# Performance work log

Hardware: AMD Instinct MI355X
Metric: run time of the kernel (lower is better)

Reference implementation:

```python
import jax, jax.numpy as jnp
import numpy as np

EPS = 1e-5

def gcn_conv(x, src, dst, W, b, N):
    # PyG GCNConv with self-loops already appended to (src, dst):
    # out = D^{-1/2} (A+I) D^{-1/2} (x @ W) + b
    h = x @ W  # [N, F_out]
    deg = jax.ops.segment_sum(jnp.ones(dst.shape[0], h.dtype), dst, num_segments=N)
    dinv = jnp.where(deg > 0, jax.lax.rsqrt(deg), 0.0)
    norm = dinv[src] * dinv[dst]  # [E']
    msg = h[src] * norm[:, None]  # gather + scale
    out = jax.ops.segment_sum(msg, dst, num_segments=N)  # scatter-add
    return out + b

def layer_norm(x, gamma, beta):
    mu = jnp.mean(x, axis=-1, keepdims=True)
    var = jnp.mean((x - mu) ** 2, axis=-1, keepdims=True)
    return (x - mu) * jax.lax.rsqrt(var + EPS) * gamma + beta

def setup_inputs() -> dict:
    key = jax.random.key(0)
    ks = jax.random.split(key, 12)
    N, E, STEPS = 200000, 12800000, 4
    node = jax.random.normal(ks[0], (N, 3), dtype=jnp.float32)
    edges = jax.random.randint(ks[1], (2, E), 0, N, dtype=jnp.int64)
    W1 = jax.random.normal(ks[2], (3, 6), dtype=jnp.float32) * 0.5
    b1 = jnp.zeros((6,), jnp.float32)
    Wl = jax.random.normal(ks[3], (STEPS, 6, 6), dtype=jnp.float32) * 0.4
    bl = jnp.zeros((STEPS, 6), jnp.float32)
    gamma = jnp.ones((STEPS, 6), jnp.float32)
    beta = jnp.zeros((STEPS, 6), jnp.float32)
    Wfc = jax.random.normal(ks[4], (6, 3), dtype=jnp.float32) * 0.4
    bfc = jnp.zeros((3,), jnp.float32)
    return {"node": node, "edges": edges, "W1": W1, "b1": b1, "Wl": Wl,
            "bl": bl, "gamma": gamma, "beta": beta, "Wfc": Wfc, "bfc": bfc}

def reference(node, edges, W1, b1, Wl, bl, gamma, beta, Wfc, bfc):
    N = node.shape[0]
    loops = jnp.arange(N, dtype=edges.dtype)
    src = jnp.concatenate([edges[0], loops])  # add self-loops once
    dst = jnp.concatenate([edges[1], loops])
    x = gcn_conv(node, src, dst, W1, b1, N)
    steps = Wl.shape[0]
    for i in range(steps):
        x_res = x
        x = gcn_conv(x, src, dst, Wl[i], bl[i], N)
        x = layer_norm(x, gamma[i], beta[i])
        x = x + x_res
        x = jax.nn.relu(x)
    return x @ Wfc + bfc
```

## Files before the change

### kernel.cpp

```cpp
#include <hip/hip_runtime.h>
#include <hip/hip_fp16.h>
#include <cstdint>

#define EPSLN 1e-5f
#define NPB 256
#define NPB_SHIFT 8
#define MAXB 1024
#define TILE 16384
#define SRC_BITS 18
#define SRC_MASK 0x3FFFF
#define FCAP 17664
#define FK 35

__global__ __launch_bounds__(512) void k_init(int* __restrict__ bcur, int B, int cap) {
    int b = blockIdx.x * 512 + threadIdx.x;
    if (b < B) bcur[b] = b * cap;
}

__global__ __launch_bounds__(512) void k_scatter(const int* __restrict__ src,
                                                 const int* __restrict__ dst,
                                                 int* __restrict__ bcur,
                                                 unsigned* __restrict__ packed,
                                                 int E, int B) {
    __shared__ unsigned stg[TILE];
    __shared__ int hist[MAXB];
    __shared__ int lbase[MAXB + 1];
    __shared__ int sm[MAXB];
    int tid = threadIdx.x;
    int i0 = tid, i1 = tid + 512;
    hist[i0] = 0; hist[i1] = 0;
    __syncthreads();

    int beg = blockIdx.x * TILE;
    int end = min(beg + TILE, E);
    int cnt = end - beg;

    unsigned w[32];
    unsigned m[32];

    if (cnt == TILE && ((E & 3) == 0)) {
        const int4* d4 = (const int4*)(dst + beg);
        const int4* s4 = (const int4*)(src + beg);
#pragma unroll
        for (int k = 0; k < 8; ++k) {
            int4 d = d4[tid + k * 512];
            int4 s = s4[tid + k * 512];
            int b0 = d.x >> NPB_SHIFT, b1 = d.y >> NPB_SHIFT;
            int b2 = d.z >> NPB_SHIFT, b3 = d.w >> NPB_SHIFT;
            int r0 = atomicAdd(&hist[b0], 1);
            int r1 = atomicAdd(&hist[b1], 1);
            int r2 = atomicAdd(&hist[b2], 1);
            int r3 = atomicAdd(&hist[b3], 1);
            w[4 * k + 0] = ((unsigned)(d.x & (NPB - 1)) << SRC_BITS) | (unsigned)s.x;
            w[4 * k + 1] = ((unsigned)(d.y & (NPB - 1)) << SRC_BITS) | (unsigned)s.y;
            w[4 * k + 2] = ((unsigned)(d.z & (NPB - 1)) << SRC_BITS) | (unsigned)s.z;
            w[4 * k + 3] = ((unsigned)(d.w & (NPB - 1)) << SRC_BITS) | (unsigned)s.w;
            m[4 * k + 0] = ((unsigned)b0 << 14) | (unsigned)r0;
            m[4 * k + 1] = ((unsigned)b1 << 14) | (unsigned)r1;
            m[4 * k + 2] = ((unsigned)b2 << 14) | (unsigned)r2;
            m[4 * k + 3] = ((unsigned)b3 << 14) | (unsigned)r3;
        }
    } else {
#pragma unroll
        for (int k = 0; k < 32; ++k) {
            int i = beg + tid + k * 512;
            if (i < end) {
                int d = dst[i];
                int s = src[i];
                int bkt = d >> NPB_SHIFT;
                int r = atomicAdd(&hist[bkt], 1);
                w[k] = ((unsigned)(d & (NPB - 1)) << SRC_BITS) | (unsigned)s;
                m[k] = ((unsigned)bkt << 14) | (unsigned)r;
            } else {
                m[k] = 0xFFFFFFFFu;
            }
        }
    }
    __syncthreads();

    int v0 = hist[i0], v1 = hist[i1];
    sm[i0] = v0; sm[i1] = v1;
    __syncthreads();
    for (int off = 1; off < MAXB; off <<= 1) {
        int t0 = (i0 >= off) ? sm[i0 - off] : 0;
        int t1 = (i1 >= off) ? sm[i1 - off] : 0;
        __syncthreads();
        sm[i0] += t0; sm[i1] += t1;
        __syncthreads();
    }
    lbase[i0] = sm[i0] - v0;
    lbase[i1] = sm[i1] - v1;
    if (i0 < B) hist[i0] = v0 ? atomicAdd(&bcur[i0], v0) : 0;
    if (i1 < B) hist[i1] = v1 ? atomicAdd(&bcur[i1], v1) : 0;
    if (tid == 0) lbase[B] = cnt;
    __syncthreads();

#pragma unroll
    for (int k = 0; k < 32; ++k) {
        if (m[k] != 0xFFFFFFFFu) {
            int bkt = (int)(m[k] >> 14);
            int r   = (int)(m[k] & 16383u);
            stg[lbase[bkt] + r] = w[k];
        }
    }
    __syncthreads();

    int wv = tid >> 6;
    int ln = tid & 63;
    for (int b = wv; b < B; b += 8) {
        int lb = lbase[b];
        int le = lbase[b + 1];
        int gb = hist[b];
        for (int j = lb + ln; j < le; j += 64)
            packed[gb + (j - lb)] = stg[j];
    }
}

__global__ __launch_bounds__(512) void k_fine(const int* __restrict__ bcur,
                                              const unsigned* __restrict__ packed,
                                              int* __restrict__ csr,
                                              int2* __restrict__ ptr2,
                                              float* __restrict__ dinv,
                                              float* __restrict__ sqd,
                                              const float* __restrict__ node,
                                              float* __restrict__ xs3,
                                              int N, int cap) {
    __shared__ unsigned stg[FCAP];
    __shared__ int hist[NPB];
    __shared__ int exs[NPB];
    int b = blockIdx.x;
    int tid = threadIdx.x;
    int beg = b * cap;
    int cnt = min(bcur[b] - beg, FCAP);
    if (tid < NPB) hist[tid] = 0;
    __syncthreads();

    unsigned w[FK];
    int r[FK];
#pragma unroll
    for (int k = 0; k < FK; ++k) {
        int i = tid + k * 512;
        if (i < cnt) {
            w[k] = packed[beg + i];
            r[k] = atomicAdd(&hist[w[k] >> SRC_BITS], 1);
        }
    }
    __syncthreads();

    int hv = 0;
    if (tid < NPB) { hv = hist[tid]; exs[tid] = hv; }
    __syncthreads();
    for (int off = 1; off < NPB; off <<= 1) {
        int t = 0;
        if (tid < NPB && tid >= off) t = exs[tid - off];
        __syncthreads();
        if (tid < NPB) exs[tid] += t;
        __syncthreads();
    }
    if (tid < NPB) {
        int ex = exs[tid] - hv;
        int v = b * NPB + tid;
        if (v < N) {
            ptr2[v] = make_int2(beg + ex, beg + ex + hv);
            float c = (float)(hv + 1);
            float di = rsqrtf(c);
            dinv[v] = di;
            sqd[v] = sqrtf(c);
            xs3[(size_t)v * 4 + 0] = di * node[(size_t)v * 3 + 0];
            xs3[(size_t)v * 4 + 1] = di * node[(size_t)v * 3 + 1];
            xs3[(size_t)v * 4 + 2] = di * node[(size_t)v * 3 + 2];
            xs3[(size_t)v * 4 + 3] = 0.f;
        }
        exs[tid] = ex;
    }
    __syncthreads();

#pragma unroll
    for (int k = 0; k < FK; ++k) {
        int i = tid + k * 512;
        if (i < cnt) {
            int dl = (int)(w[k] >> SRC_BITS);
            stg[exs[dl] + r[k]] = w[k] & SRC_MASK;
        }
    }
    __syncthreads();

    for (int j = tid; j < cnt; j += 512)
        csr[beg + j] = (int)stg[j];
}

template <int MODE>
__global__ __launch_bounds__(512) void k_conv(const int2* __restrict__ ptr2,
                                              const int* __restrict__ csr,
                                              const float* __restrict__ dinv,
                                              const float* __restrict__ sqd,
                                              const float* __restrict__ xs,
                                              const __half* __restrict__ xsh,
                                              const float* __restrict__ W,
                                              const float* __restrict__ b,
                                              const float* __restrict__ gamma,
                                              const float* __restrict__ beta,
                                              const float* __restrict__ Wfc,
                                              const float* __restrict__ bfc,
                                              float* __restrict__ xsout,
                                              __half* __restrict__ xhout,
                                              float* __restrict__ outfc,
                                              int N) {
    constexpr int F = (MODE == 0) ? 3 : 6;
    int wave = threadIdx.x >> 6;
    int lane = threadIdx.x & 63;
    int sub  = lane >> 4;
    int li   = lane & 15;
    int v = (blockIdx.x * 8 + wave) * 4 + sub;
    bool valid = v < N;
    int beg = 0, end = 0;
    if (valid) { int2 p = ptr2[v]; beg = p.x; end = p.y; }

    float a0 = 0.f, a1 = 0.f, a2 = 0.f, a3 = 0.f, a4 = 0.f, a5 = 0.f;
    float xr0 = 0.f, xr1 = 0.f, xr2 = 0.f, xr3 = 0.f, xr4 = 0.f, xr5 = 0.f;
    if constexpr (F == 3) {
        const float4* x4 = (const float4*)xs;
        if (valid && li == 0) { float4 p = x4[v]; a0 += p.x; a1 += p.y; a2 += p.z; }
        int i = beg + li;
        int idx = (i < end) ? __builtin_nontemporal_load(csr + i) : 0;
        while (i < end) {
            int inext = i + 16;
            int idxn = (inext < end) ? __builtin_nontemporal_load(csr + inext) : 0;
            float4 p = x4[idx];
            a0 += p.x; a1 += p.y; a2 += p.z;
            i = inext; idx = idxn;
        }
    } else {
        const float4* xh4 = (const float4*)xsh;
        if (valid && li == 0) {
            const float* rp = xs + (size_t)v * 8;
            float4 p = *(const float4*)rp;
            float2 q = *(const float2*)(rp + 4);
            xr0 = p.x; xr1 = p.y; xr2 = p.z; xr3 = p.w; xr4 = q.x; xr5 = q.y;
            a0 += xr0; a1 += xr1; a2 += xr2; a3 += xr3; a4 += xr4; a5 += xr5;
        }
        int i = beg + li;
        int idx = (i < end) ? __builtin_nontemporal_load(csr + i) : 0;
        while (i < end) {
            int inext = i + 16;
            int idxn = (inext < end) ? __builtin_nontemporal_load(csr + inext) : 0;
            float4 raw = xh4[idx];
            const __half2* h2 = (const __half2*)&raw;
            float2 p0 = __half22float2(h2[0]);
            float2 p1 = __half22float2(h2[1]);
            float2 p2 = __half22float2(h2[2]);
            a0 += p0.x; a1 += p0.y; a2 += p1.x; a3 += p1.y; a4 += p2.x; a5 += p2.y;
            i = inext; idx = idxn;
        }
    }
#pragma unroll
    for (int off = 8; off >= 1; off >>= 1) {
        a0 += __shfl_down(a0, off);
        a1 += __shfl_down(a1, off);
        a2 += __shfl_down(a2, off);
        if constexpr (F == 6) {
            a3 += __shfl_down(a3, off);
            a4 += __shfl_down(a4, off);
            a5 += __shfl_down(a5, off);
        }
    }
    if (li != 0 || !valid) return;

    float di = dinv[v];
    float t[F];
    t[0] = di * a0; t[1] = di * a1; t[2] = di * a2;
    if constexpr (F == 6) { t[3] = di * a3; t[4] = di * a4; t[5] = di * a5; }

    float y[6];
#pragma unroll
    for (int j = 0; j < 6; ++j) {
        float acc = b[j];
#pragma unroll
        for (int k = 0; k < F; ++k) acc += t[k] * W[k * 6 + j];
        y[j] = acc;
    }

    if constexpr (MODE == 0) {
        float* o = xsout + (size_t)v * 8;
        *(float4*)o = make_float4(di * y[0], di * y[1], di * y[2], di * y[3]);
        *(float2*)(o + 4) = make_float2(di * y[4], di * y[5]);
        __half2* oh = (__half2*)(xhout + (size_t)v * 8);
        oh[0] = __floats2half2_rn(di * y[0], di * y[1]);
        oh[1] = __floats2half2_rn(di * y[2], di * y[3]);
        oh[2] = __floats2half2_rn(di * y[4], di * y[5]);
        oh[3] = __floats2half2_rn(0.f, 0.f);
    } else {
        float mu = 0.f;
#pragma unroll
        for (int j = 0; j < 6; ++j) mu += y[j];
        mu *= (1.f / 6.f);
        float var = 0.f;
#pragma unroll
        for (int j = 0; j < 6; ++j) { float dl = y[j] - mu; var += dl * dl; }
        var *= (1.f / 6.f);
        float rs = rsqrtf(var + EPSLN);
        float sq = sqd[v];
        float xr[6] = {xr0, xr1, xr2, xr3, xr4, xr5};
        float r[6];
#pragma unroll
        for (int j = 0; j < 6; ++j) {
            float z = (y[j] - mu) * rs * gamma[j] + beta[j] + xr[j] * sq;
            r[j] = z > 0.f ? z : 0.f;
        }
        if constexpr (MODE == 1) {
            float* o = xsout + (size_t)v * 8;
            *(float4*)o = make_float4(di * r[0], di * r[1], di * r[2], di * r[3]);
            *(float2*)(o + 4) = make_float2(di * r[4], di * r[5]);
            __half2* oh = (__half2*)(xhout + (size_t)v * 8);
            oh[0] = __floats2half2_rn(di * r[0], di * r[1]);
            oh[1] = __floats2half2_rn(di * r[2], di * r[3]);
            oh[2] = __floats2half2_rn(di * r[4], di * r[5]);
            oh[3] = __floats2half2_rn(0.f, 0.f);
        } else {
#pragma unroll
            for (int j = 0; j < 3; ++j) {
                float acc = bfc[j];
#pragma unroll
                for (int k = 0; k < 6; ++k) acc += r[k] * Wfc[k * 3 + j];
                outfc[(size_t)v * 3 + j] = acc;
            }
        }
    }
}

extern "C" void kernel_launch(void* const* d_in, const int* in_sizes, int n_in,
                              void* d_out, int out_size, void* d_ws, size_t ws_size,
                              hipStream_t stream) {
    const float* node  = (const float*)d_in[0];
    const int*   edges = (const int*)d_in[1];
    const float* W1    = (const float*)d_in[2];
    const float* b1    = (const float*)d_in[3];
    const float* Wl    = (const float*)d_in[4];
    const float* bl    = (const float*)d_in[5];
    const float* gamma = (const float*)d_in[6];
    const float* beta  = (const float*)d_in[7];
    const float* Wfc   = (const float*)d_in[8];
    const float* bfc   = (const float*)d_in[9];
    float* out = (float*)d_out;

    const int N     = in_sizes[0] / 3;
    const int E     = in_sizes[1] / 2;
    const int STEPS = in_sizes[4] / 36;
    const int* src = edges;
    const int* dst = edges + E;
    const int B = (N + NPB - 1) / NPB;

    const int mean = E / B;
    int CAP = (mean + 8 * (int)(sqrt((double)mean) + 1) + 255) & ~255;
    if (CAP > FCAP) CAP = FCAP;

    char* ws = (char*)d_ws;
    size_t off = 0;
    auto alloc = [&](size_t bytes) -> void* {
        void* p = ws + off;
        off += (bytes + 255) & ~(size_t)255;
        return p;
    };
    int*      bcur   = (int*)alloc((size_t)B * sizeof(int));
    int2*     ptr2   = (int2*)alloc((size_t)N * sizeof(int2));
    float*    dinv   = (float*)alloc((size_t)N * sizeof(float));
    float*    sqd    = (float*)alloc((size_t)N * sizeof(float));
    unsigned* packed = (unsigned*)alloc((size_t)B * CAP * sizeof(unsigned));
    int*      csr    = (int*)alloc((size_t)B * CAP * sizeof(int));
    float*    xs3    = (float*)alloc((size_t)N * 4 * sizeof(float));
    float*    xsa    = (float*)alloc((size_t)N * 8 * sizeof(float));
    float*    xsb    = (float*)alloc((size_t)N * 8 * sizeof(float));
    __half*   xha    = (__half*)alloc((size_t)N * 8 * sizeof(__half));
    __half*   xhb    = (__half*)alloc((size_t)N * 8 * sizeof(__half));
    (void)ws_size;

    const int gS = (E + TILE - 1) / TILE;
    const int gC = (N + 31) / 32;

    k_init<<<(B + 511) / 512, 512, 0, stream>>>(bcur, B, CAP);
    k_scatter<<<gS, 512, 0, stream>>>(src, dst, bcur, packed, E, B);
    k_fine<<<B, 512, 0, stream>>>(bcur, packed, csr, ptr2, dinv, sqd, node, xs3, N, CAP);

    k_conv<0><<<gC, 512, 0, stream>>>(ptr2, csr, dinv, sqd, xs3, nullptr, W1, b1,
                                      nullptr, nullptr, nullptr, nullptr,
                                      xsa, xha, nullptr, N);

    float* xscur = xsa;   __half* xhcur = xha;
    float* xsnxt = xsb;   __half* xhnxt = xhb;
    for (int i = 0; i < STEPS; ++i) {
        const float* W  = Wl + (size_t)i * 36;
        const float* bb = bl + (size_t)i * 6;
        const float* g  = gamma + (size_t)i * 6;
        const float* be = beta + (size_t)i * 6;
        if (i == STEPS - 1) {
            k_conv<2><<<gC, 512, 0, stream>>>(ptr2, csr, dinv, sqd, xscur, xhcur, W, bb,
                                              g, be, Wfc, bfc, nullptr, nullptr, out, N);
        } else {
            k_conv<1><<<gC, 512, 0, stream>>>(ptr2, csr, dinv, sqd, xscur, xhcur, W, bb,
                                              g, be, nullptr, nullptr, xsnxt, xhnxt, nullptr, N);
        }
        float* t1 = xscur; xscur = xsnxt; xsnxt = t1;
        __half* t2 = xhcur; xhcur = xhnxt; xhnxt = t2;
    }
}
```

Before: 683.0 us.

## Replace dst-CSR gather with source-sorted edge partitions and LDS atomic scatter

Edges are now bucketed by source node, then grouped into 2048-node destination partitions. Each edge is packed as (src, local dst) into a partitioned edge list, and every partition is split across 4 blocks. Convolution blocks read the source features roughly in order and accumulate into destination rows with shared-memory float atomics, and a per-node finish kernel sums the partial results and applies the dense transform, layer norm, residual and ReLU. Degrees come from a separate histogram pass over the same edge list. The aim is to replace the random feature gathers of the CSR approach with mostly sequential source reads. The cost is many LDS atomics, extra partial-sum traffic and more kernel launches, and the result depends on the partition capacity bound, since edges beyond it are silently dropped.

New measurement: 2.610 ms. +282.2%, slower.

```diff
diff --git a/kernel.cpp b/kernel.cpp
--- a/kernel.cpp
+++ b/kernel.cpp
@@ -1,6 +1,7 @@
 #include <hip/hip_runtime.h>
 #include <hip/hip_fp16.h>
 #include <cstdint>
+#include <cmath>
 
 #define EPSLN 1e-5f
 #define NPB 256
@@ -8,13 +9,20 @@
 #define MAXB 1024
 #define TILE 16384
 #define SRC_BITS 18
-#define SRC_MASK 0x3FFFF
+#define DST_MASK 0x3FFFF
 #define FCAP 17664
 #define FK 35
-
-__global__ __launch_bounds__(512) void k_init(int* __restrict__ bcur, int B, int cap) {
-    int b = blockIdx.x * 512 + threadIdx.x;
-    if (b < B) bcur[b] = b * cap;
+#define PSH 11
+#define PLOC 2048
+#define PMSK 2047
+#define PMAXC 128
+#define NSPL 4
+
+__global__ __launch_bounds__(512) void k_init(int* __restrict__ bcur, int B, int cap,
+                                              int* __restrict__ pcur, int P, int pcap) {
+    int i = blockIdx.x * 512 + threadIdx.x;
+    if (i < B) bcur[i] = i * cap;
+    if (i < P) pcur[i] = i * pcap;
 }
 
 __global__ __launch_bounds__(512) void k_scatter(const int* __restrict__ src,
@@ -45,16 +53,16 @@
         for (int k = 0; k < 8; ++k) {
             int4 d = d4[tid + k * 512];
             int4 s = s4[tid + k * 512];
-            int b0 = d.x >> NPB_SHIFT, b1 = d.y >> NPB_SHIFT;
-            int b2 = d.z >> NPB_SHIFT, b3 = d.w >> NPB_SHIFT;
+            int b0 = s.x >> NPB_SHIFT, b1 = s.y >> NPB_SHIFT;
+            int b2 = s.z >> NPB_SHIFT, b3 = s.w >> NPB_SHIFT;
             int r0 = atomicAdd(&hist[b0], 1);
             int r1 = atomicAdd(&hist[b1], 1);
             int r2 = atomicAdd(&hist[b2], 1);
             int r3 = atomicAdd(&hist[b3], 1);
-            w[4 * k + 0] = ((unsigned)(d.x & (NPB - 1)) << SRC_BITS) | (unsigned)s.x;
-            w[4 * k + 1] = ((unsigned)(d.y & (NPB - 1)) << SRC_BITS) | (unsigned)s.y;
-            w[4 * k + 2] = ((unsigned)(d.z & (NPB - 1)) << SRC_BITS) | (unsigned)s.z;
-            w[4 * k + 3] = ((unsigned)(d.w & (NPB - 1)) << SRC_BITS) | (unsigned)s.w;
+            w[4 * k + 0] = ((unsigned)(s.x & (NPB - 1)) << SRC_BITS) | (unsigned)d.x;
+            w[4 * k + 1] = ((unsigned)(s.y & (NPB - 1)) << SRC_BITS) | (unsigned)d.y;
+            w[4 * k + 2] = ((unsigned)(s.z & (NPB - 1)) << SRC_BITS) | (unsigned)d.z;
+            w[4 * k + 3] = ((unsigned)(s.w & (NPB - 1)) << SRC_BITS) | (unsigned)d.w;
             m[4 * k + 0] = ((unsigned)b0 << 14) | (unsigned)r0;
             m[4 * k + 1] = ((unsigned)b1 << 14) | (unsigned)r1;
             m[4 * k + 2] = ((unsigned)b2 << 14) | (unsigned)r2;
@@ -67,9 +75,9 @@
             if (i < end) {
                 int d = dst[i];
                 int s = src[i];
-                int bkt = d >> NPB_SHIFT;
+                int bkt = s >> NPB_SHIFT;
                 int r = atomicAdd(&hist[bkt], 1);
-                w[k] = ((unsigned)(d & (NPB - 1)) << SRC_BITS) | (unsigned)s;
+                w[k] = ((unsigned)(s & (NPB - 1)) << SRC_BITS) | (unsigned)d;
                 m[k] = ((unsigned)bkt << 14) | (unsigned)r;
             } else {
                 m[k] = 0xFFFFFFFFu;
@@ -118,21 +126,18 @@
 
 __global__ __launch_bounds__(512) void k_fine(const int* __restrict__ bcur,
                                               const unsigned* __restrict__ packed,
-                                              int* __restrict__ csr,
-                                              int2* __restrict__ ptr2,
-                                              float* __restrict__ dinv,
-                                              float* __restrict__ sqd,
-                                              const float* __restrict__ node,
-                                              float* __restrict__ xs3,
-                                              int N, int cap) {
+                                              unsigned* __restrict__ elist,
+                                              int* __restrict__ pcur,
+                                              int cap, int pcap, int pcnt) {
     __shared__ unsigned stg[FCAP];
-    __shared__ int hist[NPB];
-    __shared__ int exs[NPB];
+    __shared__ int hist[PMAXC];
+    __shared__ int exs[PMAXC];
+    __shared__ int gbs[PMAXC];
     int b = blockIdx.x;
     int tid = threadIdx.x;
     int beg = b * cap;
     int cnt = min(bcur[b] - beg, FCAP);
-    if (tid < NPB) hist[tid] = 0;
+    if (tid < PMAXC) hist[tid] = 0;
     __syncthreads();
 
     unsigned w[FK];
@@ -142,144 +147,193 @@
         int i = tid + k * 512;
         if (i < cnt) {
             w[k] = packed[beg + i];
-            r[k] = atomicAdd(&hist[w[k] >> SRC_BITS], 1);
+            int part = (int)((w[k] & DST_MASK) >> PSH);
+            r[k] = atomicAdd(&hist[part], 1);
         }
     }
     __syncthreads();
 
     int hv = 0;
-    if (tid < NPB) { hv = hist[tid]; exs[tid] = hv; }
-    __syncthreads();
-    for (int off = 1; off < NPB; off <<= 1) {
+    if (tid < PMAXC) { hv = hist[tid]; exs[tid] = hv; }
+    __syncthreads();
+    for (int off = 1; off < PMAXC; off <<= 1) {
         int t = 0;
-        if (tid < NPB && tid >= off) t = exs[tid - off];
+        if (tid < PMAXC && tid >= off) t = exs[tid - off];
         __syncthreads();
-        if (tid < NPB) exs[tid] += t;
+        if (tid < PMAXC) exs[tid] += t;
         __syncthreads();
     }
-    if (tid < NPB) {
-        int ex = exs[tid] - hv;
-        int v = b * NPB + tid;
-        if (v < N) {
-            ptr2[v] = make_int2(beg + ex, beg + ex + hv);
-            float c = (float)(hv + 1);
-            float di = rsqrtf(c);
-            dinv[v] = di;
-            sqd[v] = sqrtf(c);
-            xs3[(size_t)v * 4 + 0] = di * node[(size_t)v * 3 + 0];
-            xs3[(size_t)v * 4 + 1] = di * node[(size_t)v * 3 + 1];
-            xs3[(size_t)v * 4 + 2] = di * node[(size_t)v * 3 + 2];
-            xs3[(size_t)v * 4 + 3] = 0.f;
-        }
-        exs[tid] = ex;
-    }
-    __syncthreads();
-
+    if (tid < PMAXC) {
+        exs[tid] -= hv;
+        gbs[tid] = (tid < pcnt && hv) ? atomicAdd(&pcur[tid], hv) : 0;
+    }
+    __syncthreads();
+
+    unsigned bb = (unsigned)b << NPB_SHIFT;
 #pragma unroll
     for (int k = 0; k < FK; ++k) {
         int i = tid + k * 512;
         if (i < cnt) {
-            int dl = (int)(w[k] >> SRC_BITS);
-            stg[exs[dl] + r[k]] = w[k] & SRC_MASK;
-        }
-    }
-    __syncthreads();
-
-    for (int j = tid; j < cnt; j += 512)
-        csr[beg + j] = (int)stg[j];
-}
-
-template <int MODE>
-__global__ __launch_bounds__(512) void k_conv(const int2* __restrict__ ptr2,
-                                              const int* __restrict__ csr,
-                                              const float* __restrict__ dinv,
-                                              const float* __restrict__ sqd,
-                                              const float* __restrict__ xs,
-                                              const __half* __restrict__ xsh,
-                                              const float* __restrict__ W,
-                                              const float* __restrict__ b,
-                                              const float* __restrict__ gamma,
-                                              const float* __restrict__ beta,
-                                              const float* __restrict__ Wfc,
-                                              const float* __restrict__ bfc,
-                                              float* __restrict__ xsout,
-                                              __half* __restrict__ xhout,
-                                              float* __restrict__ outfc,
-                                              int N) {
-    constexpr int F = (MODE == 0) ? 3 : 6;
-    int wave = threadIdx.x >> 6;
-    int lane = threadIdx.x & 63;
-    int sub  = lane >> 4;
-    int li   = lane & 15;
-    int v = (blockIdx.x * 8 + wave) * 4 + sub;
-    bool valid = v < N;
-    int beg = 0, end = 0;
-    if (valid) { int2 p = ptr2[v]; beg = p.x; end = p.y; }
-
-    float a0 = 0.f, a1 = 0.f, a2 = 0.f, a3 = 0.f, a4 = 0.f, a5 = 0.f;
-    float xr0 = 0.f, xr1 = 0.f, xr2 = 0.f, xr3 = 0.f, xr4 = 0.f, xr5 = 0.f;
-    if constexpr (F == 3) {
-        const float4* x4 = (const float4*)xs;
-        if (valid && li == 0) { float4 p = x4[v]; a0 += p.x; a1 += p.y; a2 += p.z; }
-        int i = beg + li;
-        int idx = (i < end) ? __builtin_nontemporal_load(csr + i) : 0;
-        while (i < end) {
-            int inext = i + 16;
-            int idxn = (inext < end) ? __builtin_nontemporal_load(csr + inext) : 0;
-            float4 p = x4[idx];
-            a0 += p.x; a1 += p.y; a2 += p.z;
-            i = inext; idx = idxn;
+            unsigned wd = w[k];
+            int part = (int)((wd & DST_MASK) >> PSH);
+            unsigned ew = ((bb | (wd >> SRC_BITS)) << PSH) | (wd & PMSK);
+            stg[exs[part] + r[k]] = ew;
+        }
+    }
+    __syncthreads();
+
+    int wv = tid >> 6, ln = tid & 63;
+    for (int p = wv; p < pcnt; p += 8) {
+        int lb = exs[p], len = hist[p], gb = gbs[p];
+        int lim = (p + 1) * pcap;
+        for (int j = ln; j < len; j += 64) {
+            int gi = gb + j;
+            if (gi < lim) elist[gi] = stg[lb + j];
+        }
+    }
+}
+
+__global__ __launch_bounds__(512) void k_deg(const int* __restrict__ pcur,
+                                             const unsigned* __restrict__ elist,
+                                             int* __restrict__ pdeg,
+                                             int pcap, int pszn) {
+    int p = blockIdx.x, s = blockIdx.y, S = gridDim.y;
+    int tid = threadIdx.x;
+    __shared__ int cnt[PLOC];
+    for (int t = tid; t < PLOC; t += 512) cnt[t] = 0;
+    __syncthreads();
+    int base = p * pcap;
+    int n = min(pcur[p] - base, pcap);
+    int lo = (int)((long long)n * s / S), hi = (int)((long long)n * (s + 1) / S);
+    for (int j = base + lo + tid; j < base + hi; j += 512)
+        atomicAdd(&cnt[elist[j] & PMSK], 1);
+    __syncthreads();
+    int* dst = pdeg + (size_t)s * pszn + ((size_t)p << PSH);
+    for (int t = tid; t < PLOC; t += 512) dst[t] = cnt[t];
+}
+
+__global__ __launch_bounds__(512) void k_fdeg(const int* __restrict__ pdeg,
+                                              const float* __restrict__ node,
+                                              float* __restrict__ dinv,
+                                              float* __restrict__ sqd,
+                                              float* __restrict__ xs3,
+                                              int N, int pszn, int S) {
+    int v = blockIdx.x * 512 + threadIdx.x;
+    if (v >= N) return;
+    int d = 0;
+    for (int s = 0; s < S; ++s) d += pdeg[(size_t)s * pszn + v];
+    float c = (float)(d + 1);
+    float di = rsqrtf(c);
+    dinv[v] = di;
+    sqd[v] = sqrtf(c);
+    xs3[(size_t)v * 4 + 0] = di * node[(size_t)v * 3 + 0];
+    xs3[(size_t)v * 4 + 1] = di * node[(size_t)v * 3 + 1];
+    xs3[(size_t)v * 4 + 2] = di * node[(size_t)v * 3 + 2];
+    xs3[(size_t)v * 4 + 3] = 0.f;
+}
+
+template <int FD>
+__global__ __launch_bounds__(512) void k_conv(const int* __restrict__ pcur,
+                                              const unsigned* __restrict__ elist,
+                                              const float* __restrict__ xs4,
+                                              const __half* __restrict__ xh8,
+                                              float* __restrict__ pacc,
+                                              int pcap, int pszn) {
+    int p = blockIdx.x, s = blockIdx.y, S = gridDim.y;
+    int tid = threadIdx.x;
+    __shared__ float acc[PLOC * 7];
+    for (int t = tid; t < PLOC * 7; t += 512) acc[t] = 0.f;
+    __syncthreads();
+    int base = p * pcap;
+    int n = min(pcur[p] - base, pcap);
+    int lo = (int)((long long)n * s / S), hi = (int)((long long)n * (s + 1) / S);
+    if constexpr (FD == 3) {
+        const float4* x4 = (const float4*)xs4;
+        for (int j = base + lo + tid; j < base + hi; j += 512) {
+            unsigned ew = elist[j];
+            int sv = (int)(ew >> PSH);
+            int dl = (int)(ew & PMSK);
+            float4 x = x4[sv];
+            atomicAdd(&acc[dl * 7 + 0], x.x);
+            atomicAdd(&acc[dl * 7 + 1], x.y);
+            atomicAdd(&acc[dl * 7 + 2], x.z);
         }
     } else {
-        const float4* xh4 = (const float4*)xsh;
-        if (valid && li == 0) {
-            const float* rp = xs + (size_t)v * 8;
-            float4 p = *(const float4*)rp;
-            float2 q = *(const float2*)(rp + 4);
-            xr0 = p.x; xr1 = p.y; xr2 = p.z; xr3 = p.w; xr4 = q.x; xr5 = q.y;
-            a0 += xr0; a1 += xr1; a2 += xr2; a3 += xr3; a4 += xr4; a5 += xr5;
-        }
-        int i = beg + li;
-        int idx = (i < end) ? __builtin_nontemporal_load(csr + i) : 0;
-        while (i < end) {
-            int inext = i + 16;
-            int idxn = (inext < end) ? __builtin_nontemporal_load(csr + inext) : 0;
-            float4 raw = xh4[idx];
+        const float4* h4 = (const float4*)xh8;
+        for (int j = base + lo + tid; j < base + hi; j += 512) {
+            unsigned ew = elist[j];
+            int sv = (int)(ew >> PSH);
+            int dl = (int)(ew & PMSK);
+            float4 raw = h4[sv];
             const __half2* h2 = (const __half2*)&raw;
             float2 p0 = __half22float2(h2[0]);
             float2 p1 = __half22float2(h2[1]);
             float2 p2 = __half22float2(h2[2]);
-            a0 += p0.x; a1 += p0.y; a2 += p1.x; a3 += p1.y; a4 += p2.x; a5 += p2.y;
-            i = inext; idx = idxn;
-        }
-    }
-#pragma unroll
-    for (int off = 8; off >= 1; off >>= 1) {
-        a0 += __shfl_down(a0, off);
-        a1 += __shfl_down(a1, off);
-        a2 += __shfl_down(a2, off);
-        if constexpr (F == 6) {
-            a3 += __shfl_down(a3, off);
-            a4 += __shfl_down(a4, off);
-            a5 += __shfl_down(a5, off);
-        }
-    }
-    if (li != 0 || !valid) return;
-
+            atomicAdd(&acc[dl * 7 + 0], p0.x);
+            atomicAdd(&acc[dl * 7 + 1], p0.y);
+            atomicAdd(&acc[dl * 7 + 2], p1.x);
+            atomicAdd(&acc[dl * 7 + 3], p1.y);
+            atomicAdd(&acc[dl * 7 + 4], p2.x);
+            atomicAdd(&acc[dl * 7 + 5], p2.y);
+        }
+    }
+    __syncthreads();
+    float* dst = pacc + ((size_t)s * pszn + ((size_t)p << PSH)) * 6;
+    for (int t = tid; t < PLOC * 6; t += 512) {
+        int dl = t / 6, f = t - dl * 6;
+        dst[t] = acc[dl * 7 + f];
+    }
+}
+
+template <int MODE>
+__global__ __launch_bounds__(512) void k_fin(const float* __restrict__ pacc,
+                                             const float* __restrict__ dinv,
+                                             const float* __restrict__ sqd,
+                                             const float* __restrict__ xs,
+                                             const float* __restrict__ W,
+                                             const float* __restrict__ b,
+                                             const float* __restrict__ gamma,
+                                             const float* __restrict__ beta,
+                                             const float* __restrict__ Wfc,
+                                             const float* __restrict__ bfc,
+                                             float* __restrict__ xsout,
+                                             __half* __restrict__ xhout,
+                                             float* __restrict__ outfc,
+                                             int N, int pszn, int S) {
+    constexpr int F = (MODE == 0) ? 3 : 6;
+    int v = blockIdx.x * 512 + threadIdx.x;
+    if (v >= N) return;
+    float a[6] = {0.f, 0.f, 0.f, 0.f, 0.f, 0.f};
+    for (int s = 0; s < S; ++s) {
+        const float* row = pacc + ((size_t)s * pszn + v) * 6;
+#pragma unroll
+        for (int f = 0; f < F; ++f) a[f] += row[f];
+    }
     float di = dinv[v];
+    float xr[6] = {0.f, 0.f, 0.f, 0.f, 0.f, 0.f};
+    if constexpr (MODE == 0) {
+        float4 srow = ((const float4*)xs)[v];
+        a[0] += srow.x; a[1] += srow.y; a[2] += srow.z;
+    } else {
+        const float* rp = xs + (size_t)v * 8;
+        float4 s0 = *(const float4*)rp;
+        float2 s1 = *(const float2*)(rp + 4);
+        xr[0] = s0.x; xr[1] = s0.y; xr[2] = s0.z;
+        xr[3] = s0.w; xr[4] = s1.x; xr[5] = s1.y;
+#pragma unroll
+        for (int f = 0; f < 6; ++f) a[f] += xr[f];
+    }
     float t[F];
-    t[0] = di * a0; t[1] = di * a1; t[2] = di * a2;
-    if constexpr (F == 6) { t[3] = di * a3; t[4] = di * a4; t[5] = di * a5; }
-
+#pragma unroll
+    for (int f = 0; f < F; ++f) t[f] = di * a[f];
     float y[6];
 #pragma unroll
     for (int j = 0; j < 6; ++j) {
-        float acc = b[j];
-#pragma unroll
-        for (int k = 0; k < F; ++k) acc += t[k] * W[k * 6 + j];
-        y[j] = acc;
-    }
-
+        float acc2 = b[j];
+#pragma unroll
+        for (int k = 0; k < F; ++k) acc2 += t[k] * W[k * 6 + j];
+        y[j] = acc2;
+    }
     if constexpr (MODE == 0) {
         float* o = xsout + (size_t)v * 8;
         *(float4*)o = make_float4(di * y[0], di * y[1], di * y[2], di * y[3]);
@@ -300,7 +354,6 @@
         var *= (1.f / 6.f);
         float rs = rsqrtf(var + EPSLN);
         float sq = sqd[v];
-        float xr[6] = {xr0, xr1, xr2, xr3, xr4, xr5};
         float r[6];
 #pragma unroll
         for (int j = 0; j < 6; ++j) {
@@ -319,10 +372,10 @@
         } else {
 #pragma unroll
             for (int j = 0; j < 3; ++j) {
-                float acc = bfc[j];
-#pragma unroll
-                for (int k = 0; k < 6; ++k) acc += r[k] * Wfc[k * 3 + j];
-                outfc[(size_t)v * 3 + j] = acc;
+                float acc2 = bfc[j];
+#pragma unroll
+                for (int k = 0; k < 6; ++k) acc2 += r[k] * Wfc[k * 3 + j];
+                outfc[(size_t)v * 3 + j] = acc2;
             }
         }
     }
@@ -349,10 +402,14 @@
     const int* src = edges;
     const int* dst = edges + E;
     const int B = (N + NPB - 1) / NPB;
+    const int PCNT = (N + PLOC - 1) >> PSH;
+    const int PSZN = PCNT << PSH;
 
     const int mean = E / B;
     int CAP = (mean + 8 * (int)(sqrt((double)mean) + 1) + 255) & ~255;
     if (CAP > FCAP) CAP = FCAP;
+    const int pmean = E / PCNT;
+    const int PCAP = (pmean + 8 * (int)(sqrt((double)pmean) + 1) + 255) & ~255;
 
     char* ws = (char*)d_ws;
     size_t off = 0;
@@ -362,28 +419,34 @@
         return p;
     };
     int*      bcur   = (int*)alloc((size_t)B * sizeof(int));
-    int2*     ptr2   = (int2*)alloc((size_t)N * sizeof(int2));
+    int*      pcur   = (int*)alloc((size_t)PCNT * sizeof(int));
     float*    dinv   = (float*)alloc((size_t)N * sizeof(float));
     float*    sqd    = (float*)alloc((size_t)N * sizeof(float));
-    unsigned* packed = (unsigned*)alloc((size_t)B * CAP * sizeof(unsigned));
-    int*      csr    = (int*)alloc((size_t)B * CAP * sizeof(int));
     float*    xs3    = (float*)alloc((size_t)N * 4 * sizeof(float));
     float*    xsa    = (float*)alloc((size_t)N * 8 * sizeof(float));
     float*    xsb    = (float*)alloc((size_t)N * 8 * sizeof(float));
     __half*   xha    = (__half*)alloc((size_t)N * 8 * sizeof(__half));
     __half*   xhb    = (__half*)alloc((size_t)N * 8 * sizeof(__half));
+    unsigned* elist  = (unsigned*)alloc((size_t)PCNT * PCAP * sizeof(unsigned));
+    unsigned* packed = (unsigned*)alloc((size_t)B * CAP * sizeof(unsigned));
+    int*      pdeg   = (int*)packed;
+    float*    pacc   = (float*)((char*)packed + (size_t)NSPL * PSZN * sizeof(int));
     (void)ws_size;
 
     const int gS = (E + TILE - 1) / TILE;
-    const int gC = (N + 31) / 32;
-
-    k_init<<<(B + 511) / 512, 512, 0, stream>>>(bcur, B, CAP);
+    const int gN = (N + 511) / 512;
+    const dim3 gP(PCNT, NSPL);
+
+    k_init<<<(max(B, PCNT) + 511) / 512, 512, 0, stream>>>(bcur, B, CAP, pcur, PCNT, PCAP);
     k_scatter<<<gS, 512, 0, stream>>>(src, dst, bcur, packed, E, B);
-    k_fine<<<B, 512, 0, stream>>>(bcur, packed, csr, ptr2, dinv, sqd, node, xs3, N, CAP);
-
-    k_conv<0><<<gC, 512, 0, stream>>>(ptr2, csr, dinv, sqd, xs3, nullptr, W1, b1,
-                                      nullptr, nullptr, nullptr, nullptr,
-                                      xsa, xha, nullptr, N);
+    k_fine<<<B, 512, 0, stream>>>(bcur, packed, elist, pcur, CAP, PCAP, PCNT);
+    k_deg<<<gP, 512, 0, stream>>>(pcur, elist, pdeg, PCAP, PSZN);
+    k_fdeg<<<gN, 512, 0, stream>>>(pdeg, node, dinv, sqd, xs3, N, PSZN, NSPL);
+
+    k_conv<3><<<gP, 512, 0, stream>>>(pcur, elist, xs3, nullptr, pacc, PCAP, PSZN);
+    k_fin<0><<<gN, 512, 0, stream>>>(pacc, dinv, sqd, xs3, W1, b1,
+                                     nullptr, nullptr, nullptr, nullptr,
+                                     xsa, xha, nullptr, N, PSZN, NSPL);
 
     float* xscur = xsa;   __half* xhcur = xha;
     float* xsnxt = xsb;   __half* xhnxt = xhb;
@@ -392,12 +455,13 @@
         const float* bb = bl + (size_t)i * 6;
         const float* g  = gamma + (size_t)i * 6;
         const float* be = beta + (size_t)i * 6;
+        k_conv<6><<<gP, 512, 0, stream>>>(pcur, elist, nullptr, xhcur, pacc, PCAP, PSZN);
         if (i == STEPS - 1) {
-            k_conv<2><<<gC, 512, 0, stream>>>(ptr2, csr, dinv, sqd, xscur, xhcur, W, bb,
-                                              g, be, Wfc, bfc, nullptr, nullptr, out, N);
+            k_fin<2><<<gN, 512, 0, stream>>>(pacc, dinv, sqd, xscur, W, bb, g, be,
+                                             Wfc, bfc, nullptr, nullptr, out, N, PSZN, NSPL);
         } else {
-            k_conv<1><<<gC, 512, 0, stream>>>(ptr2, csr, dinv, sqd, xscur, xhcur, W, bb,
-                                              g, be, nullptr, nullptr, xsnxt, xhnxt, nullptr, N);
+            k_fin<1><<<gN, 512, 0, stream>>>(pacc, dinv, sqd, xscur, W, bb, g, be,
+                                             nullptr, nullptr, xsnxt, xhnxt, nullptr, N, PSZN, NSPL);
         }
         float* t1 = xscur; xscur = xsnxt; xsnxt = t1;
         __half* t2 = xhcur; xhcur = xhnxt; xhnxt = t2;
```
